# Performance work log

Measured on AMD Instinct MI355X. Metric: run time of the kernel, lower is better.

Reference implementation:

```python
import jax, jax.numpy as jnp
import numpy as np

B, N, D = 4, 4096, 256

def setup_inputs() -> dict:
    key = jax.random.key(0)
    ks = jax.random.split(key, 5)
    s = 1.0 / np.sqrt(D)
    return {
        'x': jax.random.normal(ks[0], (B, N, D), jnp.float32),
        'Wq': jax.random.normal(ks[1], (D, D), jnp.float32) * s,
        'bq': jnp.zeros((D,), jnp.float32),
        'Wk': jax.random.normal(ks[2], (D, D), jnp.float32) * s,
        'bk': jnp.zeros((D,), jnp.float32),
        'Wv': jax.random.normal(ks[3], (D, D), jnp.float32) * s,
        'bv': jnp.zeros((D,), jnp.float32),
        'Wfc': jax.random.normal(ks[4], (D, D), jnp.float32) * s,
        'bfc': jnp.zeros((D,), jnp.float32),
    }

def reference(x, Wq, bq, Wk, bk, Wv, bv, Wfc, bfc):
    # Linear layers: y = x @ W^T + b (torch nn.Linear convention)
    q = jnp.einsum('bnd,ed->bne', x, Wq) + bq
    k = jnp.einsum('bnd,ed->bne', x, Wk) + bk
    v = jnp.einsum('bnd,ed->bne', x, Wv) + bv
    # NOTE: source has no 1/sqrt(d) scaling — keep it faithful.
    attn = jnp.einsum('bnd,bmd->bnm', q, k)          # [B, N, N]
    attn = jax.nn.softmax(attn, axis=-1)
    out = jnp.einsum('bnm,bmd->bnd', attn, v)        # [B, N, D]
    out = jnp.einsum('bnd,ed->bne', out, Wfc) + bfc
    return out
```

## Files before the change

kernel.cpp:

```cpp
#include <hip/hip_runtime.h>
#include <stdint.h>

#define B_ 4
#define N_ 4096
#define D_ 256
#define M_ (B_*N_)

typedef _Float16 f16;
typedef _Float16 f16x8 __attribute__((ext_vector_type(8)));
typedef float    f32x4  __attribute__((ext_vector_type(4)));
typedef float    f32x16 __attribute__((ext_vector_type(16)));

#define MFMA16(A,B,C) __builtin_amdgcn_mfma_f32_16x16x32_f16(A,B,C,0,0,0)
#define MFMA32(A,B,C) __builtin_amdgcn_mfma_f32_32x32x16_f16(A,B,C,0,0,0)

#define QH_OFF   0u
#define KH_OFF   8388608u
#define VT_OFF   16777216u
#define WFCH_OFF 25165824u
#define WQS_OFF  25296896u
#define WKS_OFF  25559040u
#define WVS_OFF  25821184u
#define OP_OFF   26083328u
#define ML_OFF   59637760u

typedef __attribute__((address_space(3))) uint32_t lds_u32;
typedef __attribute__((address_space(1))) const uint32_t g_u32;

__device__ __forceinline__ void stage16(const f16* g, f16* lbase) {
    __builtin_amdgcn_global_load_lds((g_u32*)g, (lds_u32*)lbase, 16, 0, 0);
}
__device__ __forceinline__ uint32_t pk2(float a, float b) {
    union { f16 h[2]; uint32_t u; } x;
    x.h[0] = (f16)a; x.h[1] = (f16)b;
    return x.u;
}

__global__ __launch_bounds__(256) void cvt_w(
    const float* __restrict__ Wq, const float* __restrict__ Wk,
    const float* __restrict__ Wv, const float* __restrict__ Wfc,
    f16* __restrict__ Wqs, f16* __restrict__ Wks, f16* __restrict__ Wvs,
    f16* __restrict__ Wfch)
{
    const int z = blockIdx.y;
    const float* W = (z==0) ? Wq : (z==1) ? Wk : (z==2) ? Wv : Wfc;
    int idx = (blockIdx.x * 256 + threadIdx.x) * 4;
    float4 v = *(const float4*)(W + idx);
    union { ushort4 u4; f16 h[4]; } hi, lo;
    float vv[4] = {v.x, v.y, v.z, v.w};
    #pragma unroll
    for (int j = 0; j < 4; j++) {
        hi.h[j] = (f16)vv[j];
        lo.h[j] = (f16)(vv[j] - (float)hi.h[j]);
    }
    if (z == 3) {
        *(ushort4*)(Wfch + idx) = hi.u4;
    } else {
        f16* Ws = (z==0) ? Wqs : (z==1) ? Wks : Wvs;
        int col = idx >> 8, k = idx & 255;
        int dc = k >> 5, c8 = (k >> 3) & 3, j = k & 7;
        int p  = c8 ^ ((col >> 2) & 3);
        int base = dc*16384 + col*32 + p*8 + j;
        *(ushort4*)(Ws + base)        = hi.u4;
        *(ushort4*)(Ws + base + 8192) = lo.u4;
    }
}

__global__ __launch_bounds__(256, 2) void proj_kernel(
    const float* __restrict__ x,
    const f16* __restrict__ Wqs, const f16* __restrict__ Wks,
    const f16* __restrict__ Wvs,
    const float* __restrict__ bq, const float* __restrict__ bk,
    const float* __restrict__ bv,
    f16* __restrict__ Qh, f16* __restrict__ Kh, f16* __restrict__ Vt)
{
    const int z = blockIdx.y;
    const f16*   Ws   = (z==0) ? Wqs : (z==1) ? Wks : Wvs;
    const float* bias = (z==0) ? bq  : (z==1) ? bk  : bv;

    __shared__ __align__(16) f16 Bs[2][16384];

    const int tid  = threadIdx.x;
    const int w    = tid >> 6;
    const int lane = tid & 63;
    const int l15  = lane & 15;
    const int q4   = lane >> 4;
    const int m0   = blockIdx.x * 64 + w * 16;
    const int rowA = m0 + l15;
    const int sw   = (l15 >> 2) & 3;

    int s8[8];
    #pragma unroll
    for (int i = 0; i < 8; i++) s8[i] = (tid + i*256) * 8;

    f32x4 acc[16];
    #pragma unroll
    for (int nt = 0; nt < 16; nt++) acc[nt] = (f32x4){0.f,0.f,0.f,0.f};

    #pragma unroll
    for (int i = 0; i < 8; i++) stage16(Ws + s8[i], &Bs[0][0] + s8[i]);
    const float* xp = x + (size_t)rowA * 256;
    float4 a0 = *(const float4*)(xp + q4*8);
    float4 a1 = *(const float4*)(xp + q4*8 + 4);

    for (int dc = 0; dc < 8; dc++) {
        const int cur = dc & 1;
        __syncthreads();
        if (dc < 7) {
            const f16* src = Ws + (size_t)(dc+1)*16384;
            f16* dst = &Bs[cur ^ 1][0];
            #pragma unroll
            for (int i = 0; i < 8; i++) stage16(src + s8[i], dst + s8[i]);
        }
        float av[8] = {a0.x,a0.y,a0.z,a0.w,a1.x,a1.y,a1.z,a1.w};
        f16x8 ah, alo;
        #pragma unroll
        for (int j = 0; j < 8; j++) {
            ah[j]  = (f16)av[j];
            alo[j] = (f16)(av[j] - (float)ah[j]);
        }
        if (dc < 7) {
            a0 = *(const float4*)(xp + (dc+1)*32 + q4*8);
            a1 = *(const float4*)(xp + (dc+1)*32 + q4*8 + 4);
        }
        const f16* Bc = &Bs[cur][0];
        #pragma unroll
        for (int nt = 0; nt < 16; nt++) {
            const f16* bp = Bc + (nt*16 + l15)*32 + ((q4 ^ sw) << 3);
            f16x8 bh = *(const f16x8*)bp;
            f16x8 bl = *(const f16x8*)(bp + 8192);
            acc[nt] = MFMA16(ah,  bl, acc[nt]);
            acc[nt] = MFMA16(alo, bh, acc[nt]);
            acc[nt] = MFMA16(ah,  bh, acc[nt]);
        }
    }

    if (z == 0) {
        #pragma unroll
        for (int nt = 0; nt < 16; nt++) {
            float bb = bias[nt*16 + l15];
            #pragma unroll
            for (int r = 0; r < 4; r++)
                Qh[(size_t)(m0 + q4*4 + r)*256 + nt*16 + l15] = (f16)(acc[nt][r] + bb);
        }
    } else if (z == 1) {
        const int cbase = (l15 >> 3);
        const int j     = l15 & 7;
        #pragma unroll
        for (int nt = 0; nt < 16; nt++) {
            float bb = bias[nt*16 + l15];
            int c = nt*2 + cbase;
            #pragma unroll
            for (int r = 0; r < 4; r++) {
                int m = m0 + q4*4 + r;
                Kh[(size_t)m*256 + (size_t)((c ^ (m & 7)) << 3) + j] = (f16)(acc[nt][r] + bb);
            }
        }
    } else {
        uint32_t* VTs = (uint32_t*)&Bs[0][0];
        const int bb_ = m0 >> 12;
        const int n0  = (blockIdx.x * 64) & 4095;
        const int mloc = w*16 + q4*4;
        const int mc   = mloc >> 3;
        __syncthreads();
        #pragma unroll
        for (int nt = 0; nt < 16; nt++) {
            int e = nt*16 + l15;
            float bv_ = bias[e];
            uint32_t w0 = pk2(acc[nt][0]+bv_, acc[nt][1]+bv_);
            uint32_t w1 = pk2(acc[nt][2]+bv_, acc[nt][3]+bv_);
            int base = e*36 + ((mc ^ (e & 7)) << 2) + ((q4*2) & 3);
            VTs[base]     = w0;
            VTs[base + 1] = w1;
        }
        __syncthreads();
        #pragma unroll
        for (int i = 0; i < 8; i++) {
            int e  = w*64 + i*8 + (lane >> 3);
            int nc = lane & 7;
            const f16* src = (const f16*)&VTs[e*36 + ((nc ^ (e & 7)) << 2)];
            f16x8 v = *(const f16x8*)src;
            *(f16x8*)(Vt + ((size_t)bb_*256 + e)*4096 + n0 + nc*8) = v;
        }
    }
}

#define MARGIN 10.0f
__global__ __launch_bounds__(256, 2) void attn_kernel(
    const f16* __restrict__ Qh, const f16* __restrict__ Kh,
    const f16* __restrict__ Vt,
    f16* __restrict__ Opart, float* __restrict__ Ml)
{
    __shared__ __align__(16) f16 SMEM[32768];
    f16* Ks = SMEM;
    f16* Vs = SMEM + 16384;

    const int combo = blockIdx.x & 15;
    const int b   = combo >> 2;
    const int sp  = combo & 3;
    const int qt  = blockIdx.x >> 4;
    const int tid  = threadIdx.x;
    const int w    = tid >> 6;
    const int lane = tid & 63;
    const int l31  = lane & 31;
    const int half = lane >> 5;
    const int qbase = qt * 128 + w * 32;
    const int vx   = (l31 >> 2) & 3;

    f16x8 qf[16];
    {
        const f16* qp = Qh + ((size_t)(b*4096 + qbase + l31))*256 + half*8;
        #pragma unroll
        for (int st = 0; st < 16; st++) qf[st] = *(const f16x8*)(qp + st*16);
    }

    f32x16 Oa[8];
    #pragma unroll
    for (int t = 0; t < 8; t++)
        #pragma unroll
        for (int r = 0; r < 16; r++) Oa[t][r] = 0.f;
    float mo = -3e38f, ls = 0.f;

    const f16* kg0 = Kh + ((size_t)(b*4096 + sp*1024)) * 256;
    const f16* vg0 = Vt + ((size_t)b*256) * 4096 + sp*1024;

    int kslot[4], voff[4];
    #pragma unroll
    for (int i = 0; i < 4; i++) {
        int s = tid + i*256;
        kslot[i] = s * 8;
        int d = s >> 2;
        int kc = (s & 3) ^ ((s >> 4) & 3);
        voff[i] = d * 4096 + kc * 8;
    }

    #pragma unroll
    for (int i = 0; i < 4; i++) stage16(kg0 + kslot[i], Ks + kslot[i]);

    f16x8 bp0, bp1;

    for (int it = 0; it < 32; it++) {
        const int cur = it & 1;
        __syncthreads();
        if (it + 1 < 32) {
            const f16* kg = kg0 + (size_t)(it+1) * 8192;
            f16* kl = Ks + (cur ^ 1) * 8192;
            #pragma unroll
            for (int i = 0; i < 4; i++) stage16(kg + kslot[i], kl + kslot[i]);
        }
        {
            const f16* vg = vg0 + it*32;
            f16* vl = Vs + cur * 8192;
            #pragma unroll
            for (int i = 0; i < 4; i++) stage16(vg + voff[i], vl + kslot[i]);
        }

        const f16* krp = Ks + cur*8192 + l31*256;
        const f16* vpp = Vs + (cur^1)*8192 + l31*32;
        f32x16 sa;
        #pragma unroll
        for (int r = 0; r < 16; r++) sa[r] = 0.f;
        if (it > 0) {
            #pragma unroll
            for (int st = 0; st < 16; st++) {
                f16x8 ka = *(const f16x8*)(krp + (((st*2 + half) ^ (lane & 7)) << 3));
                sa = MFMA32(ka, qf[st], sa);
                int t = st >> 1, kh = st & 1;
                f16x8 va = *(const f16x8*)(vpp + t*1024 + (((half + kh*2) ^ vx) << 3));
                Oa[t] = MFMA32(va, kh ? bp1 : bp0, Oa[t]);
            }
        } else {
            #pragma unroll
            for (int st = 0; st < 16; st++) {
                f16x8 ka = *(const f16x8*)(krp + (((st*2 + half) ^ (lane & 7)) << 3));
                sa = MFMA32(ka, qf[st], sa);
            }
        }

        float tm = sa[0];
        #pragma unroll
        for (int r = 1; r < 16; r++) tm = fmaxf(tm, sa[r]);
        if (__any(tm > mo + MARGIN)) {
            float tmq = fmaxf(tm, __shfl_xor(tm, 32));
            float mn = fmaxf(mo, tmq);
            float al = __expf(mo - mn);
            mo = mn; ls *= al;
            #pragma unroll
            for (int t = 0; t < 8; t++)
                #pragma unroll
                for (int r = 0; r < 16; r++) Oa[t][r] *= al;
        }
        float p[16];
        #pragma unroll
        for (int r = 0; r < 16; r++) { p[r] = __expf(sa[r] - mo); ls += p[r]; }

        #pragma unroll
        for (int kh = 0; kh < 2; kh++) {
            uint32_t lo0 = pk2(p[8*kh+0], p[8*kh+1]);
            uint32_t lo1 = pk2(p[8*kh+2], p[8*kh+3]);
            uint32_t hi0 = pk2(p[8*kh+4], p[8*kh+5]);
            uint32_t hi1 = pk2(p[8*kh+6], p[8*kh+7]);
            uint32_t s0 = half ? lo0 : hi0;
            uint32_t s1 = half ? lo1 : hi1;
            uint32_t r0 = __shfl_xor(s0, 32);
            uint32_t r1 = __shfl_xor(s1, 32);
            uint32_t k0 = half ? hi0 : lo0;
            uint32_t k1 = half ? hi1 : lo1;
            union { uint32_t u[4]; f16x8 v; } bb;
            bb.u[0] = half ? r0 : k0;
            bb.u[1] = half ? r1 : k1;
            bb.u[2] = half ? k0 : r0;
            bb.u[3] = half ? k1 : r1;
            if (kh == 0) bp0 = bb.v; else bp1 = bb.v;
        }
    }

    __syncthreads();
    {
        const f16* vpp = Vs + 8192 + l31*32;
        #pragma unroll
        for (int t = 0; t < 8; t++) {
            #pragma unroll
            for (int kh = 0; kh < 2; kh++) {
                f16x8 va = *(const f16x8*)(vpp + t*1024 + (((half + kh*2) ^ vx) << 3));
                Oa[t] = MFMA32(va, kh ? bp1 : bp0, Oa[t]);
            }
        }
    }
    __syncthreads();

    float l = ls + __shfl_xor(ls, 32);
    float inv = 1.0f / l;
    f16* tb = SMEM + w * 8192;
    #pragma unroll
    for (int t = 0; t < 8; t++) {
        #pragma unroll
        for (int rp = 0; rp < 8; rp++) {
            int r0 = rp * 2;
            int d  = (r0 & 3) + 8*(r0 >> 2) + 4*half + t*32;
            int c  = d >> 3, j = d & 7;
            uint32_t wv = pk2(Oa[t][r0]*inv, Oa[t][r0+1]*inv);
            *(uint32_t*)(tb + l31*256 + ((c ^ (l31 & 7)) << 3) + (j & 6)) = wv;
        }
    }
    f16* opb = Opart + ((size_t)sp*M_ + b*4096 + qbase) * 256;
    #pragma unroll
    for (int i = 0; i < 16; i++) {
        int q = (i & 3)*8 + (lane >> 3);
        int c = (i >> 2)*8 + (lane & 7);
        f16x8 v = *(const f16x8*)(tb + q*256 + ((c ^ (q & 7)) << 3));
        *(f16x8*)(opb + (size_t)q*256 + c*8) = v;
    }
    if (half == 0) {
        size_t mrow = (size_t)sp*M_ + b*4096 + qbase + l31;
        Ml[mrow*2]     = mo;
        Ml[mrow*2 + 1] = l;
    }
}

__global__ __launch_bounds__(256) void merge_fc_kernel(
    const f16* __restrict__ Opart, const float* __restrict__ Ml,
    const f16* __restrict__ Wfch, const float* __restrict__ bfc,
    float* __restrict__ out)
{
    const int tid  = threadIdx.x;
    const int w    = tid >> 6;
    const int lane = tid & 63;
    const int l15  = lane & 15;
    const int q4   = lane >> 4;
    const int m0   = blockIdx.x * 64 + w * 16;

    const int rowA = m0 + l15;
    float mv[4], lv[4];
    #pragma unroll
    for (int p = 0; p < 4; p++) {
        mv[p] = Ml[((size_t)p*M_ + rowA)*2];
        lv[p] = Ml[((size_t)p*M_ + rowA)*2 + 1];
    }
    float mm = fmaxf(fmaxf(mv[0], mv[1]), fmaxf(mv[2], mv[3]));
    float cw[4], den = 0.f;
    #pragma unroll
    for (int p = 0; p < 4; p++) { cw[p] = __expf(mv[p] - mm) * lv[p]; den += cw[p]; }
    float inv = 1.0f / den;
    #pragma unroll
    for (int p = 0; p < 4; p++) cw[p] *= inv;

    f16x8 af[8];
    #pragma unroll
    for (int dc = 0; dc < 8; dc++) {
        float v[8] = {};
        #pragma unroll
        for (int p = 0; p < 4; p++) {
            f16x8 o = *(const f16x8*)(Opart + ((size_t)p*M_ + rowA)*256 + q4*8 + dc*32);
            #pragma unroll
            for (int j = 0; j < 8; j++) v[j] += cw[p] * (float)o[j];
        }
        f16x8 h;
        #pragma unroll
        for (int j = 0; j < 8; j++) h[j] = (f16)v[j];
        af[dc] = h;
    }

    f32x4 acc[16];
    #pragma unroll
    for (int nt = 0; nt < 16; nt++) acc[nt] = (f32x4){0.f,0.f,0.f,0.f};
    #pragma unroll
    for (int dc = 0; dc < 8; dc++) {
        #pragma unroll
        for (int nt = 0; nt < 16; nt++) {
            f16x8 bf = *(const f16x8*)(Wfch + (size_t)(nt*16 + l15)*256 + dc*32 + q4*8);
            acc[nt] = MFMA16(af[dc], bf, acc[nt]);
        }
    }
    #pragma unroll
    for (int nt = 0; nt < 16; nt++) {
        float bias = bfc[nt*16 + l15];
        #pragma unroll
        for (int r = 0; r < 4; r++)
            out[(size_t)(m0 + q4*4 + r) * 256 + nt*16 + l15] = acc[nt][r] + bias;
    }
}

extern "C" void kernel_launch(void* const* d_in, const int* in_sizes, int n_in,
                              void* d_out, int out_size, void* d_ws, size_t ws_size,
                              hipStream_t stream)
{
    const float* x   = (const float*)d_in[0];
    const float* Wq  = (const float*)d_in[1];
    const float* bq  = (const float*)d_in[2];
    const float* Wk  = (const float*)d_in[3];
    const float* bk  = (const float*)d_in[4];
    const float* Wv  = (const float*)d_in[5];
    const float* bv  = (const float*)d_in[6];
    const float* Wfc = (const float*)d_in[7];
    const float* bfc = (const float*)d_in[8];
    float* out = (float*)d_out;

    char* ws = (char*)d_ws;
    f16*   Qh    = (f16*)(ws + QH_OFF);
    f16*   Kh    = (f16*)(ws + KH_OFF);
    f16*   Vt    = (f16*)(ws + VT_OFF);
    f16*   Wfch  = (f16*)(ws + WFCH_OFF);
    f16*   Wqs   = (f16*)(ws + WQS_OFF);
    f16*   Wks   = (f16*)(ws + WKS_OFF);
    f16*   Wvs   = (f16*)(ws + WVS_OFF);
    f16*   Opart = (f16*)(ws + OP_OFF);
    float* Ml    = (float*)(ws + ML_OFF);

    cvt_w<<<dim3(64, 4), 256, 0, stream>>>(Wq, Wk, Wv, Wfc, Wqs, Wks, Wvs, Wfch);
    proj_kernel<<<dim3(256, 3), 256, 0, stream>>>(x, Wqs, Wks, Wvs, bq, bk, bv, Qh, Kh, Vt);
    attn_kernel<<<512, 256, 0, stream>>>(Qh, Kh, Vt, Opart, Ml);
    merge_fc_kernel<<<256, 256, 0, stream>>>(Opart, Ml, Wfch, bfc, out);
}
```

Baseline: 218.4 us.

## Stage swizzled Wfc tiles through double-buffered LDS in merge_fc kernel

Wfc is now converted into a chunked, XOR-swizzled layout so the merge_fc kernel can copy each 32-column chunk into a double-buffered shared-memory tile and read B fragments from LDS instead of global memory. The Opart loads and weighted merge are interleaved with the MFMA loop, prefetching the next chunk's partials, and launch bounds now target two blocks per CU. The aim is to cut repeated global/L2 reads of Wfc and hide load latency, at the cost of 32KB LDS per block and a barrier per chunk.

Measured after the change: 207.3 us. 1.05x faster.

```diff
diff --git a/kernel.cpp b/kernel.cpp
--- a/kernel.cpp
+++ b/kernel.cpp
@@ -53,13 +53,13 @@
         hi.h[j] = (f16)vv[j];
         lo.h[j] = (f16)(vv[j] - (float)hi.h[j]);
     }
+    int col = idx >> 8, k = idx & 255;
+    int dc = k >> 5, c8 = (k >> 3) & 3, j = k & 7;
+    int p  = c8 ^ ((col >> 2) & 3);
     if (z == 3) {
-        *(ushort4*)(Wfch + idx) = hi.u4;
+        *(ushort4*)(Wfch + dc*8192 + col*32 + p*8 + j) = hi.u4;
     } else {
         f16* Ws = (z==0) ? Wqs : (z==1) ? Wks : Wvs;
-        int col = idx >> 8, k = idx & 255;
-        int dc = k >> 5, c8 = (k >> 3) & 3, j = k & 7;
-        int p  = c8 ^ ((col >> 2) & 3);
         int base = dc*16384 + col*32 + p*8 + j;
         *(ushort4*)(Ws + base)        = hi.u4;
         *(ushort4*)(Ws + base + 8192) = lo.u4;
@@ -358,19 +358,26 @@
     }
 }
 
-__global__ __launch_bounds__(256) void merge_fc_kernel(
+__global__ __launch_bounds__(256, 2) void merge_fc_kernel(
     const f16* __restrict__ Opart, const float* __restrict__ Ml,
-    const f16* __restrict__ Wfch, const float* __restrict__ bfc,
+    const f16* __restrict__ Wfci, const float* __restrict__ bfc,
     float* __restrict__ out)
 {
+    __shared__ __align__(16) f16 Bs[2][8192];
+
     const int tid  = threadIdx.x;
     const int w    = tid >> 6;
     const int lane = tid & 63;
     const int l15  = lane & 15;
     const int q4   = lane >> 4;
     const int m0   = blockIdx.x * 64 + w * 16;
-
     const int rowA = m0 + l15;
+    const int sw   = (l15 >> 2) & 3;
+
+    int s4[4];
+    #pragma unroll
+    for (int i = 0; i < 4; i++) s4[i] = (tid + i*256) * 8;
+
     float mv[4], lv[4];
     #pragma unroll
     for (int p = 0; p < 4; p++) {
@@ -381,35 +388,48 @@
     float cw[4], den = 0.f;
     #pragma unroll
     for (int p = 0; p < 4; p++) { cw[p] = __expf(mv[p] - mm) * lv[p]; den += cw[p]; }
-    float inv = 1.0f / den;
-    #pragma unroll
-    for (int p = 0; p < 4; p++) cw[p] *= inv;
-
-    f16x8 af[8];
-    #pragma unroll
+    float invd = 1.0f / den;
+    #pragma unroll
+    for (int p = 0; p < 4; p++) cw[p] *= invd;
+
+    #pragma unroll
+    for (int i = 0; i < 4; i++) stage16(Wfci + s4[i], &Bs[0][0] + s4[i]);
+    const f16* opb = Opart + (size_t)rowA*256 + q4*8;
+    f16x8 of[4];
+    #pragma unroll
+    for (int p = 0; p < 4; p++) of[p] = *(const f16x8*)(opb + (size_t)p*M_*256);
+
+    f32x4 acc[16];
+    #pragma unroll
+    for (int nt = 0; nt < 16; nt++) acc[nt] = (f32x4){0.f,0.f,0.f,0.f};
+
     for (int dc = 0; dc < 8; dc++) {
+        const int cur = dc & 1;
+        __syncthreads();
+        if (dc < 7) {
+            const f16* src = Wfci + (size_t)(dc+1)*8192;
+            f16* dst = &Bs[cur ^ 1][0];
+            #pragma unroll
+            for (int i = 0; i < 4; i++) stage16(src + s4[i], dst + s4[i]);
+        }
         float v[8] = {};
         #pragma unroll
-        for (int p = 0; p < 4; p++) {
-            f16x8 o = *(const f16x8*)(Opart + ((size_t)p*M_ + rowA)*256 + q4*8 + dc*32);
-            #pragma unroll
-            for (int j = 0; j < 8; j++) v[j] += cw[p] * (float)o[j];
-        }
-        f16x8 h;
-        #pragma unroll
-        for (int j = 0; j < 8; j++) h[j] = (f16)v[j];
-        af[dc] = h;
-    }
-
-    f32x4 acc[16];
-    #pragma unroll
-    for (int nt = 0; nt < 16; nt++) acc[nt] = (f32x4){0.f,0.f,0.f,0.f};
-    #pragma unroll
-    for (int dc = 0; dc < 8; dc++) {
+        for (int p = 0; p < 4; p++)
+            #pragma unroll
+            for (int j = 0; j < 8; j++) v[j] += cw[p] * (float)of[p][j];
+        f16x8 af;
+        #pragma unroll
+        for (int j = 0; j < 8; j++) af[j] = (f16)v[j];
+        if (dc < 7) {
+            #pragma unroll
+            for (int p = 0; p < 4; p++)
+                of[p] = *(const f16x8*)(opb + (size_t)p*M_*256 + (dc+1)*32);
+        }
+        const f16* Bc = &Bs[cur][0];
         #pragma unroll
         for (int nt = 0; nt < 16; nt++) {
-            f16x8 bf = *(const f16x8*)(Wfch + (size_t)(nt*16 + l15)*256 + dc*32 + q4*8);
-            acc[nt] = MFMA16(af[dc], bf, acc[nt]);
+            f16x8 bf = *(const f16x8*)(Bc + (nt*16 + l15)*32 + ((q4 ^ sw) << 3));
+            acc[nt] = MFMA16(af, bf, acc[nt]);
         }
     }
     #pragma unroll
```
